# Performance work log

Hardware: AMD Instinct MI355X
Metric: run time of the kernel (lower is better)

Reference implementation:

```python
import jax, jax.numpy as jnp
import numpy as np

N, E, H, NH, RBF = 20000, 200000, 128, 8, 64
HD = H // NH
CUT_HI = 5.0


def _ln(t, s, b, eps=1e-6):
    mu = t.mean(-1, keepdims=True)
    var = ((t - mu) ** 2).mean(-1, keepdims=True)
    return (t - mu) * jax.lax.rsqrt(var + eps) * s + b


def _cutoff(w):
    # cosine cutoff, cutoff_lower = 0
    return 0.5 * (jnp.cos(w * (jnp.pi / CUT_HI)) + 1.0) * (w < CUT_HI)


def _xavier(k, fi, fo):
    lim = float(np.sqrt(6.0 / (fi + fo)))
    return jax.random.uniform(k, (fi, fo), minval=-lim, maxval=lim, dtype=jnp.float32)


def setup_inputs() -> dict:
    key = jax.random.key(0)
    ks = jax.random.split(key, 16)
    return {
        "x": jax.random.normal(ks[0], (N, H), jnp.float32),
        "vec": jax.random.normal(ks[1], (N, 3, H), jnp.float32),
        "edge_weight": jax.random.uniform(ks[2], (E, 1), jnp.float32) * 6.0,
        "edge_attr": jax.random.uniform(ks[3], (E, RBF), jnp.float32),
        "edge_vec": jax.random.normal(ks[4], (E, 3), jnp.float32),
        "senders": jax.random.randint(ks[5], (E,), 0, N, jnp.int32),
        "receivers": jax.random.randint(ks[6], (E,), 0, N, jnp.int32),
        "ln_s": jnp.ones((H,), jnp.float32), "ln_b": jnp.zeros((H,), jnp.float32),
        "Wq": _xavier(ks[7], H, H), "bq": jnp.zeros((H,), jnp.float32),
        "Wk": _xavier(ks[8], H, H), "bk": jnp.zeros((H,), jnp.float32),
        "Wv": _xavier(ks[9], H, 3 * H), "bv": jnp.zeros((3 * H,), jnp.float32),
        "Wvec": _xavier(ks[10], H, 3 * H),
        "Wdk": _xavier(ks[11], RBF, H), "bdk": jnp.zeros((H,), jnp.float32),
        "Wdv": _xavier(ks[12], RBF, 3 * H), "bdv": jnp.zeros((3 * H,), jnp.float32),
        "Wo": _xavier(ks[13], H, 3 * H), "bo": jnp.zeros((3 * H,), jnp.float32),
        "qln_s": jnp.ones((HD,), jnp.float32), "qln_b": jnp.zeros((HD,), jnp.float32),
        "kln_s": jnp.ones((HD,), jnp.float32), "kln_b": jnp.zeros((HD,), jnp.float32),
    }


def reference(x, vec, edge_weight, edge_attr, edge_vec, senders, receivers,
              ln_s, ln_b, Wq, bq, Wk, bk, Wv, bv, Wvec, Wdk, bdk, Wdv, bdv,
              Wo, bo, qln_s, qln_b, kln_s, kln_b):
    act = jax.nn.silu
    n = x.shape[0]
    xn = _ln(x, ln_s, ln_b)                                    # [N,H]
    q = _ln((xn @ Wq + bq).reshape(n, NH, HD), qln_s, qln_b)   # [N,h,d]
    k = _ln((xn @ Wk + bk).reshape(n, NH, HD), kln_s, kln_b)   # [N,h,d]
    v = (xn @ Wv + bv).reshape(n, NH, 3 * HD)                  # [N,h,3d]
    vp = vec @ Wvec                                            # [N,3,3H]
    vec1, vec2, vec3 = jnp.split(vp, 3, axis=-1)               # [N,3,H] each
    vec_dot = (vec1 * vec2).sum(axis=1)                        # [N,H]
    vec_h = vec.reshape(n, 3, NH, HD)                          # [N,3,h,d]
    dk = act(edge_attr @ Wdk + bdk).reshape(-1, NH, HD)        # [E,h,d]
    dv = act(edge_attr @ Wdv + bdv).reshape(-1, NH, 3 * HD)    # [E,h,3d]
    # message
    attn = (q[receivers] * k[senders] * dk).sum(axis=-1)       # [E,h]
    attn = act(attn) * _cutoff(edge_weight)                    # [E,h]
    v_j = v[senders] * dv                                      # [E,h,3d]
    xm, m1, m2 = jnp.split(v_j, 3, axis=2)                     # [E,h,d]
    xm = xm * attn[:, :, None]                                 # [E,h,d]
    vec_m = vec_h[senders] * m1[:, None] + m2[:, None] * edge_vec[:, :, None, None]  # [E,3,h,d]
    # aggregate
    x_agg = jax.ops.segment_sum(xm, receivers, num_segments=n).reshape(n, H)
    vec_agg = jax.ops.segment_sum(vec_m, receivers, num_segments=n).reshape(n, 3, H)
    o1, o2, o3 = jnp.split(x_agg @ Wo + bo, 3, axis=1)         # [N,H] each
    dvec = vec3 * o1[:, None] + vec_agg                        # [N,3,H]
    dx = vec_dot * o2 + o3                                     # [N,H]
    return (dx, dvec)
```

## Files before the change

### kernel.cpp

```cpp
#include <hip/hip_runtime.h>
#include <stdint.h>

#define NN 20000
#define NE 200000

typedef __attribute__((ext_vector_type(8))) short bf16x8;
typedef __attribute__((ext_vector_type(4))) float f32x4;

__device__ __forceinline__ float bf2f(uint32_t u) {
  union { uint32_t i; float f; } v; v.i = u << 16; return v.f;
}
__device__ __forceinline__ uint16_t f2bf(float f) {
  union { float f; uint32_t i; } v; v.f = f;
  return (uint16_t)((v.i + 0x7fffu + ((v.i >> 16) & 1u)) >> 16);
}
__device__ __forceinline__ uint32_t pk2(float lo, float hi) {
  return (uint32_t)f2bf(lo) | ((uint32_t)f2bf(hi) << 16);
}
__device__ __forceinline__ float siluf(float x) { return x / (1.f + __expf(-x)); }
__device__ __forceinline__ float prod2(uint32_t q2, uint32_t k2, uint32_t d2) {
  return bf2f(q2 & 0xffffu) * bf2f(k2 & 0xffffu) * bf2f(d2 & 0xffffu)
       + bf2f(q2 >> 16) * bf2f(k2 >> 16) * bf2f(d2 >> 16);
}

__global__ void k_prep(const float* __restrict__ Wq, const float* __restrict__ Wk,
                       const float* __restrict__ Wv, const float* __restrict__ Wvec,
                       const float* __restrict__ Wdk, const float* __restrict__ Wdv,
                       const float* __restrict__ Wo, const float* __restrict__ bq,
                       const float* __restrict__ bk, const float* __restrict__ bv,
                       const float* __restrict__ bdk, const float* __restrict__ bdv,
                       uint16_t* __restrict__ WTqkv, uint16_t* __restrict__ WTvec,
                       uint16_t* __restrict__ WTdkv2, uint16_t* __restrict__ WTo,
                       float* __restrict__ Bqkv, float* __restrict__ Bdkv2) {
  int idx = blockIdx.x * 256 + threadIdx.x;
  if (idx < 81920) {
    int j = idx;
    float v;
    if (j < 16384)      { int c = j >> 7, k = j & 127; v = Wq[k * 128 + c]; }
    else if (j < 32768) { j -= 16384; int c = j >> 7, k = j & 127; v = Wk[k * 128 + c]; }
    else                { j -= 32768; int c = j >> 7, k = j & 127; v = Wv[k * 384 + c]; }
    WTqkv[idx] = f2bf(v);
    return;
  }
  idx -= 81920;
  if (idx < 49152) {
    int c = idx >> 7, k = idx & 127;
    WTvec[idx] = f2bf(Wvec[k * 384 + c]);
    return;
  }
  idx -= 49152;
  if (idx < 32768) {
    int rr = idx >> 6, k = idx & 63;
    float v;
    if (rr < 128) v = Wdk[k * 128 + rr];
    else {
      int j = rr - 128, p = j >> 7, hd = j & 127;
      int c = (hd >> 4) * 48 + p * 16 + (hd & 15);
      v = Wdv[k * 384 + c];
    }
    WTdkv2[idx] = f2bf(v);
    return;
  }
  idx -= 32768;
  if (idx < 49152) {
    int c = idx >> 7, k = idx & 127;
    WTo[idx] = f2bf(Wo[k * 384 + c]);
    return;
  }
  idx -= 49152;
  if (idx < 640) Bqkv[idx] = (idx < 128) ? bq[idx] : ((idx < 256) ? bk[idx - 128] : bv[idx - 256]);
  else if (idx < 1152) {
    int t = idx - 640;
    if (t < 128) Bdkv2[t] = bdk[t];
    else {
      int j = t - 128, p = j >> 7, hd = j & 127;
      Bdkv2[t] = bdv[(hd >> 4) * 48 + p * 16 + (hd & 15)];
    }
  }
}

__global__ void k_node_pre(const float* __restrict__ x, const float* __restrict__ s,
                           const float* __restrict__ b, const float* __restrict__ vec,
                           uint16_t* __restrict__ xn_b, uint16_t* __restrict__ vec_b) {
  if (blockIdx.x < 5000) {
    int gt = blockIdx.x * 256 + threadIdx.x;
    int node = gt >> 6, lane = gt & 63;
    if (node >= NN) return;
    const float* row = x + (size_t)node * 128;
    float2 v = *(const float2*)&row[lane * 2];
    float sum = v.x + v.y, sq = v.x * v.x + v.y * v.y;
    #pragma unroll
    for (int off = 32; off; off >>= 1) { sum += __shfl_xor(sum, off); sq += __shfl_xor(sq, off); }
    float mu = sum * (1.f / 128.f);
    float var = sq * (1.f / 128.f) - mu * mu;
    float rs = rsqrtf(var + 1e-6f);
    float o0 = (v.x - mu) * rs * s[lane * 2] + b[lane * 2];
    float o1 = (v.y - mu) * rs * s[lane * 2 + 1] + b[lane * 2 + 1];
    ((uint32_t*)xn_b)[(size_t)node * 64 + lane] = pk2(o0, o1);
  } else {
    int i = (blockIdx.x - 5000) * 256 + threadIdx.x;
    if (i >= NN * 3 * 64) return;
    float2 v = ((const float2*)vec)[i];
    ((uint32_t*)vec_b)[i] = pk2(v.x, v.y);
  }
}

__global__ void k_cast_bf16(const float* __restrict__ src, uint16_t* __restrict__ dst, int npairs) {
  int i = blockIdx.x * 256 + threadIdx.x;
  if (i >= npairs) return;
  float2 v = ((const float2*)src)[i];
  ((uint32_t*)dst)[i] = pk2(v.x, v.y);
}

__global__ void k_hist(const int* __restrict__ rcv, int* __restrict__ deg) {
  int e = blockIdx.x * 256 + threadIdx.x;
  if (e < NE) atomicAdd(&deg[rcv[e]], 1);
}

__global__ void k_scan1(const int* __restrict__ deg, int* __restrict__ bsum) {
  __shared__ int ws[4];
  int i = blockIdx.x * 256 + threadIdx.x;
  int x = (i < NN) ? deg[i] : 0;
  #pragma unroll
  for (int d = 32; d; d >>= 1) x += __shfl_xor(x, d);
  if ((threadIdx.x & 63) == 0) ws[threadIdx.x >> 6] = x;
  __syncthreads();
  if (threadIdx.x == 0) bsum[blockIdx.x] = ws[0] + ws[1] + ws[2] + ws[3];
}

__global__ void k_scan2(int* __restrict__ bsum, int nb, int* __restrict__ off) {
  int lane = threadIdx.x;
  int carry = 0;
  for (int base = 0; base < nb; base += 64) {
    int i = base + lane;
    int x = (i < nb) ? bsum[i] : 0;
    int v = x;
    #pragma unroll
    for (int d = 1; d < 64; d <<= 1) { int y = __shfl_up(v, d); if (lane >= d) v += y; }
    if (i < nb) bsum[i] = carry + v - x;
    carry += __shfl(v, 63);
  }
  if (lane == 0) off[NN] = carry;
}

__global__ void k_scan3(const int* __restrict__ deg, const int* __restrict__ bsum,
                        int* __restrict__ off, int* __restrict__ cur) {
  __shared__ int ws[4];
  int t = threadIdx.x, lane = t & 63, w = t >> 6;
  int i = blockIdx.x * 256 + t;
  int x = (i < NN) ? deg[i] : 0;
  int v = x;
  #pragma unroll
  for (int d = 1; d < 64; d <<= 1) { int y = __shfl_up(v, d); if (lane >= d) v += y; }
  if (lane == 63) ws[w] = v;
  __syncthreads();
  int wadd = 0;
  for (int j = 0; j < w; j++) wadd += ws[j];
  int excl = bsum[blockIdx.x] + wadd + v - x;
  if (i < NN) { off[i] = excl; cur[i] = excl; }
}

__global__ void k_scatter(const int* __restrict__ rcv, int* __restrict__ cur,
                          int* __restrict__ perm) {
  int e = blockIdx.x * 256 + threadIdx.x;
  if (e >= NE) return;
  int pos = atomicAdd(&cur[rcv[e]], 1);
  perm[pos] = e;
}

__global__ void k_permute(const int* __restrict__ perm, const int* __restrict__ snd,
                          const int* __restrict__ rcv, const float* __restrict__ ew,
                          const float* __restrict__ evec, int* __restrict__ sndp,
                          int* __restrict__ rcvp, float4* __restrict__ edata) {
  int i = blockIdx.x * 256 + threadIdx.x;
  if (i >= NE) return;
  int e = perm[i];
  sndp[i] = snd[e];
  rcvp[i] = rcv[e];
  float w = ew[e];
  float cut = (w < 5.f) ? 0.5f * (__cosf(w * 0.628318530717958648f) + 1.f) : 0.f;
  edata[i] = make_float4(evec[e * 3], evec[e * 3 + 1], evec[e * 3 + 2], cut);
}

template <int KTOT, bool OUT_BF16, bool SILU>
__global__ __launch_bounds__(256) void k_gemm(const uint16_t* __restrict__ A,
                                              const uint16_t* __restrict__ BT,
                                              const float* __restrict__ bias,
                                              void* __restrict__ Cout, int M, int Fo) {
  __shared__ __align__(16) uint16_t As[128 * 72];
  __shared__ __align__(16) uint16_t Bs[128 * 72];
  int t = threadIdx.x;
  int l = t & 63;
  int row0 = blockIdx.y * 128, col0 = blockIdx.x * 128;
  int wm = ((t >> 6) >> 1) * 64, wn = ((t >> 6) & 1) * 64;
  f32x4 acc[4][4] = {};
  for (int kt = 0; kt < KTOT; kt += 64) {
    __syncthreads();
    #pragma unroll
    for (int i = 0; i < 4; i++) {
      int c = i * 256 + t;
      int row = c >> 3, ko = (c & 7) * 8;
      uint4 av = make_uint4(0u, 0u, 0u, 0u);
      int gr = row0 + row;
      if (gr < M) av = *(const uint4*)&A[(size_t)gr * KTOT + kt + ko];
      *(uint4*)&As[row * 72 + ko] = av;
      uint4 bw = *(const uint4*)&BT[(size_t)(col0 + row) * KTOT + kt + ko];
      *(uint4*)&Bs[row * 72 + ko] = bw;
    }
    __syncthreads();
    #pragma unroll
    for (int kk = 0; kk < 64; kk += 32) {
      bf16x8 af[4], bfr[4];
      #pragma unroll
      for (int mf = 0; mf < 4; mf++)
        af[mf] = *(const bf16x8*)&As[(wm + mf * 16 + (l & 15)) * 72 + (l >> 4) * 8 + kk];
      #pragma unroll
      for (int nf = 0; nf < 4; nf++)
        bfr[nf] = *(const bf16x8*)&Bs[(wn + nf * 16 + (l & 15)) * 72 + (l >> 4) * 8 + kk];
      #pragma unroll
      for (int mf = 0; mf < 4; mf++)
        #pragma unroll
        for (int nf = 0; nf < 4; nf++)
          acc[mf][nf] = __builtin_amdgcn_mfma_f32_16x16x32_bf16(af[mf], bfr[nf], acc[mf][nf], 0, 0, 0);
    }
  }
  float* Cf = (float*)Cout;
  uint16_t* Cb = (uint16_t*)Cout;
  #pragma unroll
  for (int mf = 0; mf < 4; mf++) {
    #pragma unroll
    for (int r = 0; r < 4; r++) {
      int grow = row0 + wm + mf * 16 + (l >> 4) * 4 + r;
      if (grow >= M) continue;
      #pragma unroll
      for (int nf = 0; nf < 4; nf++) {
        int gcol = col0 + wn + nf * 16 + (l & 15);
        float v = acc[mf][nf][r];
        if (bias) v += bias[gcol];
        if (SILU) v = siluf(v);
        if (OUT_BF16) Cb[(size_t)grow * Fo + gcol] = f2bf(v);
        else          Cf[(size_t)grow * Fo + gcol] = v;
      }
    }
  }
}

__global__ void k_headln(const uint16_t* __restrict__ qkv, const float* __restrict__ qs,
                         const float* __restrict__ qb, const float* __restrict__ ks,
                         const float* __restrict__ kb, uint16_t* __restrict__ out) {
  int idx = blockIdx.x * 256 + threadIdx.x;
  if (idx >= NN * 16) return;
  int n = idx >> 4, ph = idx & 15, part = ph >> 3, h = ph & 7;
  const uint16_t* src = qkv + (size_t)n * 640 + part * 128 + h * 16;
  float v[16], sum = 0.f;
  #pragma unroll
  for (int i = 0; i < 16; i++) { v[i] = bf2f(src[i]); sum += v[i]; }
  float mu = sum * (1.f / 16.f), var = 0.f;
  #pragma unroll
  for (int i = 0; i < 16; i++) { float dd = v[i] - mu; var += dd * dd; }
  float rs = rsqrtf(var * (1.f / 16.f) + 1e-6f);
  const float* sc = part ? ks : qs;
  const float* bb = part ? kb : qb;
  uint16_t* dst = out + (size_t)n * 256 + part * 128 + h * 16;
  #pragma unroll
  for (int i = 0; i < 16; i++) dst[i] = f2bf((v[i] - mu) * rs * sc[i] + bb[i]);
}

__device__ __forceinline__ void mfma_cb(const uint16_t* As, const uint16_t* __restrict__ BT2,
                                        int cb, int wn, int l, f32x4 acc[4][2]) {
  #pragma unroll
  for (int kk = 0; kk < 2; kk++) {
    bf16x8 af[4];
    #pragma unroll
    for (int mf = 0; mf < 4; mf++)
      af[mf] = *(const bf16x8*)&As[(mf * 16 + (l & 15)) * 68 + (l >> 4) * 8 + kk * 32];
    #pragma unroll
    for (int nf = 0; nf < 2; nf++) {
      bf16x8 bv = *(const bf16x8*)&BT2[(size_t)(cb * 128 + wn + nf * 16 + (l & 15)) * 64 +
                                       (l >> 4) * 8 + kk * 32];
      #pragma unroll
      for (int mf = 0; mf < 4; mf++)
        acc[mf][nf] = __builtin_amdgcn_mfma_f32_16x16x32_bf16(af[mf], bv, acc[mf][nf], 0, 0, 0);
    }
  }
}

__device__ __forceinline__ void silu_store(uint16_t* mt, const float* bias_l, int cb,
                                           int wn, int l, f32x4 acc[4][2]) {
  #pragma unroll
  for (int mf = 0; mf < 4; mf++)
    #pragma unroll
    for (int r = 0; r < 4; r++) {
      int row = mf * 16 + (l >> 4) * 4 + r;
      #pragma unroll
      for (int nf = 0; nf < 2; nf++) {
        int c = wn + nf * 16 + (l & 15);
        mt[row * 140 + c] = f2bf(siluf(acc[mf][nf][r] + bias_l[cb * 128 + c]));
      }
    }
}

__global__ __launch_bounds__(256) void k_edge_all(
    const float* __restrict__ ea, const int* __restrict__ perm,
    const int* __restrict__ sndp, const int* __restrict__ rcvp,
    const int* __restrict__ off, const float4* __restrict__ edata,
    const uint16_t* __restrict__ WT2, const float* __restrict__ Bd2,
    const uint16_t* __restrict__ qk_b, const uint16_t* __restrict__ qkv_b,
    const uint16_t* __restrict__ vec_b, float* __restrict__ xagg,
    float* __restrict__ vecagg) {
  __shared__ __align__(16) uint16_t As[64 * 68];
  __shared__ __align__(16) uint16_t mt1[64 * 140];
  __shared__ __align__(16) uint16_t mt2[64 * 140];
  __shared__ float attn_l[64 * 8];
  __shared__ float bias_l[512];
  __shared__ int sndl[64], rcvl[64], lo_g[64], hi_g[64];
  __shared__ float4 ed4[64];

  int e0 = blockIdx.x * 64;
  int t = threadIdx.x, l = t & 63, wn = (t >> 6) * 32;

  if (t < 64) {
    int e = e0 + t;
    int s = sndp[e], r = rcvp[e];
    sndl[t] = s; rcvl[t] = r;
    lo_g[t] = off[r]; hi_g[t] = off[r + 1];
    ed4[t] = edata[e];
  }
  bias_l[t] = Bd2[t];
  bias_l[t + 256] = Bd2[t + 256];
  {
    int row = t >> 2, qo = (t & 3) * 16;
    int pe = perm[e0 + row];
    const float* src = ea + (size_t)pe * 64 + qo;
    float4 f0 = *(const float4*)src;
    float4 f1 = *(const float4*)(src + 4);
    float4 f2 = *(const float4*)(src + 8);
    float4 f3 = *(const float4*)(src + 12);
    uint4 o0, o1;
    o0.x = pk2(f0.x, f0.y); o0.y = pk2(f0.z, f0.w);
    o0.z = pk2(f1.x, f1.y); o0.w = pk2(f1.z, f1.w);
    o1.x = pk2(f2.x, f2.y); o1.y = pk2(f2.z, f2.w);
    o1.z = pk2(f3.x, f3.y); o1.w = pk2(f3.z, f3.w);
    *(uint4*)&As[row * 68 + qo] = o0;
    *(uint4*)&As[row * 68 + qo + 8] = o1;
  }
  __syncthreads();

  { f32x4 acc[4][2] = {}; mfma_cb(As, WT2, 0, wn, l, acc); silu_store(mt1, bias_l, 0, wn, l, acc); }
  __syncthreads();

  #pragma unroll
  for (int pass = 0; pass < 2; pass++) {
    int task = pass * 256 + t;
    int el = task >> 3, h = task & 7;
    int rn = rcvl[el], sn = sndl[el];
    const uint32_t* qp = (const uint32_t*)(qk_b + (size_t)rn * 256 + h * 16);
    const uint32_t* kp = (const uint32_t*)(qk_b + (size_t)sn * 256 + 128 + h * 16);
    const uint32_t* dp = (const uint32_t*)&mt1[el * 140 + h * 16];
    float dot = 0.f;
    #pragma unroll
    for (int j = 0; j < 8; j++) dot += prod2(qp[j], kp[j], dp[j]);
    attn_l[el * 8 + h] = siluf(dot) * ed4[el].w;
  }
  __syncthreads();

  { f32x4 acc[4][2] = {}; mfma_cb(As, WT2, 1, wn, l, acc); silu_store(mt1, bias_l, 1, wn, l, acc); }
  __syncthreads();

  {
    int col = t & 127, half = t >> 7;
    int h0 = half * 32, h1 = h0 + 32;
    int voff = 256 + (col >> 4) * 48 + (col & 15);
    float accx = 0.f;
    #pragma unroll 4
    for (int i = h0; i < h1; i++) {
      int n = rcvl[i];
      float m = bf2f(mt1[i * 140 + col]);
      float a = attn_l[i * 8 + (col >> 4)];
      float v0 = bf2f(qkv_b[(size_t)sndl[i] * 640 + voff]);
      accx += v0 * m * a;
      if (i == h1 - 1 || rcvl[i + 1] != n) {
        float* dst = &xagg[(size_t)n * 128 + col];
        if (lo_g[i] >= e0 + h0 && hi_g[i] <= e0 + h1) *dst = accx;
        else atomicAdd(dst, accx);
        accx = 0.f;
      }
    }
  }
  __syncthreads();

  { f32x4 acc[4][2] = {}; mfma_cb(As, WT2, 2, wn, l, acc); silu_store(mt1, bias_l, 2, wn, l, acc); }
  { f32x4 acc[4][2] = {}; mfma_cb(As, WT2, 3, wn, l, acc); silu_store(mt2, bias_l, 3, wn, l, acc); }
  __syncthreads();

  {
    int col = t & 127, half = t >> 7;
    int h0 = half * 32, h1 = h0 + 32;
    int v1o = 256 + (col >> 4) * 48 + 16 + (col & 15);
    float a0 = 0.f, a1 = 0.f, a2 = 0.f;
    #pragma unroll 4
    for (int i = h0; i < h1; i++) {
      int n = rcvl[i];
      int s = sndl[i];
      float m1d = bf2f(mt1[i * 140 + col]);
      float m2d = bf2f(mt2[i * 140 + col]);
      const uint16_t* vb = qkv_b + (size_t)s * 640 + v1o;
      float mm1 = bf2f(vb[0]) * m1d;
      float mm2 = bf2f(vb[16]) * m2d;
      const uint16_t* vv = vec_b + (size_t)s * 384 + col;
      float4 ev = ed4[i];
      a0 += bf2f(vv[0])   * mm1 + ev.x * mm2;
      a1 += bf2f(vv[128]) * mm1 + ev.y * mm2;
      a2 += bf2f(vv[256]) * mm1 + ev.z * mm2;
      if (i == h1 - 1 || rcvl[i + 1] != n) {
        float* d0 = &vecagg[((size_t)n * 3 + 0) * 128 + col];
        float* d1 = &vecagg[((size_t)n * 3 + 1) * 128 + col];
        float* d2 = &vecagg[((size_t)n * 3 + 2) * 128 + col];
        if (lo_g[i] >= e0 + h0 && hi_g[i] <= e0 + h1) { *d0 = a0; *d1 = a1; *d2 = a2; }
        else { atomicAdd(d0, a0); atomicAdd(d1, a1); atomicAdd(d2, a2); }
        a0 = a1 = a2 = 0.f;
      }
    }
  }
}

__global__ void k_final(const float* __restrict__ o, const uint16_t* __restrict__ vp,
                        float* __restrict__ dx, float* __restrict__ dvec) {
  int idx = blockIdx.x * 256 + threadIdx.x;
  if (idx >= NN * 128) return;
  int n = idx >> 7, j = idx & 127;
  const float* op = o + (size_t)n * 384;
  float o1 = op[j], o2 = op[128 + j], o3 = op[256 + j];
  const uint16_t* vpn = vp + (size_t)n * 3 * 384;
  float vd = 0.f;
  #pragma unroll
  for (int c = 0; c < 3; c++)
    vd += bf2f(vpn[c * 384 + j]) * bf2f(vpn[c * 384 + 128 + j]);
  dx[idx] = vd * o2 + o3;
  #pragma unroll
  for (int c = 0; c < 3; c++) {
    size_t vi = ((size_t)n * 3 + c) * 128 + j;
    dvec[vi] = bf2f(vpn[c * 384 + 256 + j]) * o1 + dvec[vi];
  }
}

static inline int cdiv_i(long long a, long long b) { return (int)((a + b - 1) / b); }

extern "C" void kernel_launch(void* const* d_in, const int* in_sizes, int n_in,
                              void* d_out, int out_size, void* d_ws, size_t ws_size,
                              hipStream_t stream) {
  const float* x    = (const float*)d_in[0];
  const float* vec  = (const float*)d_in[1];
  const float* ew   = (const float*)d_in[2];
  const float* ea   = (const float*)d_in[3];
  const float* evec = (const float*)d_in[4];
  const int*   snd  = (const int*)d_in[5];
  const int*   rcv  = (const int*)d_in[6];
  const float* ln_s = (const float*)d_in[7];
  const float* ln_b = (const float*)d_in[8];
  const float* Wq = (const float*)d_in[9];   const float* bq = (const float*)d_in[10];
  const float* Wk = (const float*)d_in[11];  const float* bk = (const float*)d_in[12];
  const float* Wv = (const float*)d_in[13];  const float* bv = (const float*)d_in[14];
  const float* Wvec = (const float*)d_in[15];
  const float* Wdk = (const float*)d_in[16]; const float* bdk = (const float*)d_in[17];
  const float* Wdv = (const float*)d_in[18]; const float* bdv = (const float*)d_in[19];
  const float* Wo = (const float*)d_in[20];  const float* bo = (const float*)d_in[21];
  const float* qln_s = (const float*)d_in[22]; const float* qln_b = (const float*)d_in[23];
  const float* kln_s = (const float*)d_in[24]; const float* kln_b = (const float*)d_in[25];
  (void)in_sizes; (void)n_in; (void)ws_size;

  uint8_t* p = (uint8_t*)d_ws;
  auto alloc = [&](size_t bytes) -> uint8_t* {
    uint8_t* r = p; p += (bytes + 255) & ~(size_t)255; return r;
  };
  uint16_t* WTqkv = (uint16_t*)alloc(640 * 128 * 2);
  float*    Bqkv  = (float*)alloc(640 * 4);
  uint16_t* WTvec = (uint16_t*)alloc(384 * 128 * 2);
  uint16_t* WTdkv = (uint16_t*)alloc(512 * 64 * 2);
  float*    Bdkv  = (float*)alloc(512 * 4);
  uint16_t* WTo   = (uint16_t*)alloc(384 * 128 * 2);
  int*      deg   = (int*)alloc(NN * 4);
  int*      off   = (int*)alloc((NN + 1) * 4);
  int*      cur   = (int*)alloc(NN * 4);
  int*      bsum  = (int*)alloc(256 * 4);
  int*      perm  = (int*)alloc((size_t)NE * 4);
  int*      sndp  = (int*)alloc((size_t)NE * 4);
  int*      rcvp  = (int*)alloc((size_t)NE * 4);
  float4*   edata = (float4*)alloc((size_t)NE * 16);
  uint16_t* xn_b  = (uint16_t*)alloc((size_t)NN * 128 * 2);
  uint16_t* qkv_b = (uint16_t*)alloc((size_t)NN * 640 * 2);
  uint16_t* qk_b  = (uint16_t*)alloc((size_t)NN * 256 * 2);
  uint16_t* vec_b = (uint16_t*)alloc((size_t)NN * 3 * 128 * 2);
  uint16_t* vp    = (uint16_t*)alloc((size_t)NN * 3 * 384 * 2);
  float*    o      = (float*)alloc((size_t)NN * 384 * 4);
  uint16_t* xagg_b = (uint16_t*)alloc((size_t)NN * 128 * 2);

  float* xagg   = (float*)d_out;
  float* vecagg = (float*)d_out + (size_t)NN * 128;

  hipMemsetAsync(d_out, 0, (size_t)out_size * 4, stream);

  k_prep<<<cdiv_i(81920 + 49152 + 32768 + 49152 + 1152, 256), 256, 0, stream>>>(
      Wq, Wk, Wv, Wvec, Wdk, Wdv, Wo, bq, bk, bv, bdk, bdv,
      WTqkv, WTvec, WTdkv, WTo, Bqkv, Bdkv);

  int NSB = cdiv_i(NN, 256);
  hipMemsetAsync(deg, 0, NN * 4, stream);
  k_hist<<<cdiv_i(NE, 256), 256, 0, stream>>>(rcv, deg);
  k_scan1<<<NSB, 256, 0, stream>>>(deg, bsum);
  k_scan2<<<1, 64, 0, stream>>>(bsum, NSB, off);
  k_scan3<<<NSB, 256, 0, stream>>>(deg, bsum, off, cur);
  k_scatter<<<cdiv_i(NE, 256), 256, 0, stream>>>(rcv, cur, perm);
  k_permute<<<cdiv_i(NE, 256), 256, 0, stream>>>(perm, snd, rcv, ew, evec, sndp, rcvp, edata);

  k_node_pre<<<5000 + cdiv_i((long long)NN * 3 * 64, 256), 256, 0, stream>>>(
      x, ln_s, ln_b, vec, xn_b, vec_b);

  { dim3 g(640 / 128, cdiv_i(NN, 128));
    k_gemm<128, true, false><<<g, 256, 0, stream>>>(xn_b, WTqkv, Bqkv, qkv_b, NN, 640); }
  k_headln<<<cdiv_i((long long)NN * 16, 256), 256, 0, stream>>>(qkv_b, qln_s, qln_b, kln_s, kln_b, qk_b);

  { dim3 g(384 / 128, cdiv_i((long long)NN * 3, 128));
    k_gemm<128, true, false><<<g, 256, 0, stream>>>(vec_b, WTvec, nullptr, vp, NN * 3, 384); }

  k_edge_all<<<NE / 64, 256, 0, stream>>>(ea, perm, sndp, rcvp, off, edata, WTdkv, Bdkv,
                                          qk_b, qkv_b, vec_b, xagg, vecagg);

  k_cast_bf16<<<cdiv_i((long long)NN * 64, 256), 256, 0, stream>>>(xagg, xagg_b, NN * 64);
  { dim3 g(384 / 128, cdiv_i(NN, 128));
    k_gemm<128, false, false><<<g, 256, 0, stream>>>(xagg_b, WTo, bo, o, NN, 384); }

  k_final<<<cdiv_i((long long)NN * 128, 256), 256, 0, stream>>>(o, vp, xagg, vecagg);
}
```

Baseline: 369.7 us.

## Pre-permute edge_attr to bf16 and process edge tile in two 32-row halves

The permute kernel now gathers edge_attr by the sorted edge order and converts it to bf16 in a contiguous buffer, so the fused edge kernel loads its A tile with coalesced 16-byte reads instead of a per-row gather of fp32 data. The edge kernel processes its 64 edges as two 32-row halves, which shrinks the message tiles in shared memory, drops the shared bias array in favor of per-lane bias registers, and should allow more blocks per CU. The cost is an extra pass that writes and rereads a 25 MB bf16 buffer, more barriers per block, and more partial-segment atomics because the aggregation segments are shorter.

```diff
diff --git a/kernel.cpp b/kernel.cpp
--- a/kernel.cpp
+++ b/kernel.cpp
@@ -168,18 +168,27 @@
   perm[pos] = e;
 }
 
-__global__ void k_permute(const int* __restrict__ perm, const int* __restrict__ snd,
-                          const int* __restrict__ rcv, const float* __restrict__ ew,
-                          const float* __restrict__ evec, int* __restrict__ sndp,
+__global__ void k_permute(const float* __restrict__ ea, const int* __restrict__ perm,
+                          const int* __restrict__ snd, const int* __restrict__ rcv,
+                          const float* __restrict__ ew, const float* __restrict__ evec,
+                          uint16_t* __restrict__ ea_perm, int* __restrict__ sndp,
                           int* __restrict__ rcvp, float4* __restrict__ edata) {
-  int i = blockIdx.x * 256 + threadIdx.x;
-  if (i >= NE) return;
+  int idx = blockIdx.x * 256 + threadIdx.x;
+  if (idx >= NE * 16) return;
+  int i = idx >> 4, j = idx & 15;
   int e = perm[i];
-  sndp[i] = snd[e];
-  rcvp[i] = rcv[e];
-  float w = ew[e];
-  float cut = (w < 5.f) ? 0.5f * (__cosf(w * 0.628318530717958648f) + 1.f) : 0.f;
-  edata[i] = make_float4(evec[e * 3], evec[e * 3 + 1], evec[e * 3 + 2], cut);
+  float4 v = *(const float4*)&ea[(size_t)e * 64 + j * 4];
+  uint2 o;
+  o.x = pk2(v.x, v.y);
+  o.y = pk2(v.z, v.w);
+  *(uint2*)&ea_perm[(size_t)i * 64 + j * 4] = o;
+  if (j == 0) {
+    sndp[i] = snd[e];
+    rcvp[i] = rcv[e];
+    float w = ew[e];
+    float cut = (w < 5.f) ? 0.5f * (__cosf(w * 0.628318530717958648f) + 1.f) : 0.f;
+    edata[i] = make_float4(evec[e * 3], evec[e * 3 + 1], evec[e * 3 + 2], cut);
+  }
 }
 
 template <int KTOT, bool OUT_BF16, bool SILU>
@@ -266,53 +275,52 @@
   for (int i = 0; i < 16; i++) dst[i] = f2bf((v[i] - mu) * rs * sc[i] + bb[i]);
 }
 
-__device__ __forceinline__ void mfma_cb(const uint16_t* As, const uint16_t* __restrict__ BT2,
-                                        int cb, int wn, int l, f32x4 acc[4][2]) {
+__device__ __forceinline__ void mfma32(const uint16_t* As, int r0,
+                                       const uint16_t* __restrict__ BT2, int cb,
+                                       int wn, int l, f32x4 acc[2][2]) {
   #pragma unroll
   for (int kk = 0; kk < 2; kk++) {
-    bf16x8 af[4];
-    #pragma unroll
-    for (int mf = 0; mf < 4; mf++)
-      af[mf] = *(const bf16x8*)&As[(mf * 16 + (l & 15)) * 68 + (l >> 4) * 8 + kk * 32];
+    bf16x8 af[2];
+    #pragma unroll
+    for (int mf = 0; mf < 2; mf++)
+      af[mf] = *(const bf16x8*)&As[(r0 + mf * 16 + (l & 15)) * 68 + (l >> 4) * 8 + kk * 32];
     #pragma unroll
     for (int nf = 0; nf < 2; nf++) {
       bf16x8 bv = *(const bf16x8*)&BT2[(size_t)(cb * 128 + wn + nf * 16 + (l & 15)) * 64 +
                                        (l >> 4) * 8 + kk * 32];
       #pragma unroll
-      for (int mf = 0; mf < 4; mf++)
+      for (int mf = 0; mf < 2; mf++)
         acc[mf][nf] = __builtin_amdgcn_mfma_f32_16x16x32_bf16(af[mf], bv, acc[mf][nf], 0, 0, 0);
     }
   }
 }
 
-__device__ __forceinline__ void silu_store(uint16_t* mt, const float* bias_l, int cb,
-                                           int wn, int l, f32x4 acc[4][2]) {
-  #pragma unroll
-  for (int mf = 0; mf < 4; mf++)
+__device__ __forceinline__ void silu_store32(uint16_t* mt, const float* bsv,
+                                             int wn, int l, f32x4 acc[2][2]) {
+  #pragma unroll
+  for (int mf = 0; mf < 2; mf++)
     #pragma unroll
     for (int r = 0; r < 4; r++) {
       int row = mf * 16 + (l >> 4) * 4 + r;
       #pragma unroll
       for (int nf = 0; nf < 2; nf++) {
         int c = wn + nf * 16 + (l & 15);
-        mt[row * 140 + c] = f2bf(siluf(acc[mf][nf][r] + bias_l[cb * 128 + c]));
+        mt[row * 140 + c] = f2bf(siluf(acc[mf][nf][r] + bsv[nf]));
       }
     }
 }
 
 __global__ __launch_bounds__(256) void k_edge_all(
-    const float* __restrict__ ea, const int* __restrict__ perm,
-    const int* __restrict__ sndp, const int* __restrict__ rcvp,
-    const int* __restrict__ off, const float4* __restrict__ edata,
-    const uint16_t* __restrict__ WT2, const float* __restrict__ Bd2,
-    const uint16_t* __restrict__ qk_b, const uint16_t* __restrict__ qkv_b,
-    const uint16_t* __restrict__ vec_b, float* __restrict__ xagg,
-    float* __restrict__ vecagg) {
+    const uint16_t* __restrict__ eap, const int* __restrict__ sndp,
+    const int* __restrict__ rcvp, const int* __restrict__ off,
+    const float4* __restrict__ edata, const uint16_t* __restrict__ WT2,
+    const float* __restrict__ Bd2, const uint16_t* __restrict__ qk_b,
+    const uint16_t* __restrict__ qkv_b, const uint16_t* __restrict__ vec_b,
+    float* __restrict__ xagg, float* __restrict__ vecagg) {
   __shared__ __align__(16) uint16_t As[64 * 68];
-  __shared__ __align__(16) uint16_t mt1[64 * 140];
-  __shared__ __align__(16) uint16_t mt2[64 * 140];
-  __shared__ float attn_l[64 * 8];
-  __shared__ float bias_l[512];
+  __shared__ __align__(16) uint16_t mtA[32 * 140];
+  __shared__ __align__(16) uint16_t mtB[32 * 140];
+  __shared__ float attn_l[32 * 8];
   __shared__ int sndl[64], rcvl[64], lo_g[64], hi_g[64];
   __shared__ float4 ed4[64];
 
@@ -321,106 +329,99 @@
 
   if (t < 64) {
     int e = e0 + t;
-    int s = sndp[e], r = rcvp[e];
-    sndl[t] = s; rcvl[t] = r;
+    int r = rcvp[e];
+    sndl[t] = sndp[e]; rcvl[t] = r;
     lo_g[t] = off[r]; hi_g[t] = off[r + 1];
     ed4[t] = edata[e];
   }
-  bias_l[t] = Bd2[t];
-  bias_l[t + 256] = Bd2[t + 256];
-  {
-    int row = t >> 2, qo = (t & 3) * 16;
-    int pe = perm[e0 + row];
-    const float* src = ea + (size_t)pe * 64 + qo;
-    float4 f0 = *(const float4*)src;
-    float4 f1 = *(const float4*)(src + 4);
-    float4 f2 = *(const float4*)(src + 8);
-    float4 f3 = *(const float4*)(src + 12);
-    uint4 o0, o1;
-    o0.x = pk2(f0.x, f0.y); o0.y = pk2(f0.z, f0.w);
-    o0.z = pk2(f1.x, f1.y); o0.w = pk2(f1.z, f1.w);
-    o1.x = pk2(f2.x, f2.y); o1.y = pk2(f2.z, f2.w);
-    o1.z = pk2(f3.x, f3.y); o1.w = pk2(f3.z, f3.w);
-    *(uint4*)&As[row * 68 + qo] = o0;
-    *(uint4*)&As[row * 68 + qo + 8] = o1;
+  #pragma unroll
+  for (int i = 0; i < 2; i++) {
+    int c = i * 256 + t;
+    int row = c >> 3, ko = (c & 7) * 8;
+    *(uint4*)&As[row * 68 + ko] = *(const uint4*)&eap[(size_t)(e0 + row) * 64 + ko];
+  }
+  float bs[4][2];
+  #pragma unroll
+  for (int cb = 0; cb < 4; cb++) {
+    bs[cb][0] = Bd2[cb * 128 + wn + (l & 15)];
+    bs[cb][1] = Bd2[cb * 128 + wn + 16 + (l & 15)];
   }
   __syncthreads();
 
-  { f32x4 acc[4][2] = {}; mfma_cb(As, WT2, 0, wn, l, acc); silu_store(mt1, bias_l, 0, wn, l, acc); }
-  __syncthreads();
-
-  #pragma unroll
-  for (int pass = 0; pass < 2; pass++) {
-    int task = pass * 256 + t;
-    int el = task >> 3, h = task & 7;
-    int rn = rcvl[el], sn = sndl[el];
-    const uint32_t* qp = (const uint32_t*)(qk_b + (size_t)rn * 256 + h * 16);
-    const uint32_t* kp = (const uint32_t*)(qk_b + (size_t)sn * 256 + 128 + h * 16);
-    const uint32_t* dp = (const uint32_t*)&mt1[el * 140 + h * 16];
-    float dot = 0.f;
-    #pragma unroll
-    for (int j = 0; j < 8; j++) dot += prod2(qp[j], kp[j], dp[j]);
-    attn_l[el * 8 + h] = siluf(dot) * ed4[el].w;
-  }
-  __syncthreads();
-
-  { f32x4 acc[4][2] = {}; mfma_cb(As, WT2, 1, wn, l, acc); silu_store(mt1, bias_l, 1, wn, l, acc); }
-  __syncthreads();
-
-  {
-    int col = t & 127, half = t >> 7;
-    int h0 = half * 32, h1 = h0 + 32;
-    int voff = 256 + (col >> 4) * 48 + (col & 15);
-    float accx = 0.f;
-    #pragma unroll 4
-    for (int i = h0; i < h1; i++) {
-      int n = rcvl[i];
-      float m = bf2f(mt1[i * 140 + col]);
-      float a = attn_l[i * 8 + (col >> 4)];
-      float v0 = bf2f(qkv_b[(size_t)sndl[i] * 640 + voff]);
-      accx += v0 * m * a;
-      if (i == h1 - 1 || rcvl[i + 1] != n) {
-        float* dst = &xagg[(size_t)n * 128 + col];
-        if (lo_g[i] >= e0 + h0 && hi_g[i] <= e0 + h1) *dst = accx;
-        else atomicAdd(dst, accx);
-        accx = 0.f;
+  #pragma unroll
+  for (int half = 0; half < 2; half++) {
+    int r0 = half * 32;
+    { f32x4 acc[2][2] = {}; mfma32(As, r0, WT2, 0, wn, l, acc); silu_store32(mtA, bs[0], wn, l, acc); }
+    __syncthreads();
+    {
+      int el = t >> 3, h = t & 7;
+      int ge = r0 + el;
+      int rn = rcvl[ge], sn = sndl[ge];
+      const uint32_t* qp = (const uint32_t*)(qk_b + (size_t)rn * 256 + h * 16);
+      const uint32_t* kp = (const uint32_t*)(qk_b + (size_t)sn * 256 + 128 + h * 16);
+      const uint32_t* dp = (const uint32_t*)&mtA[el * 140 + h * 16];
+      float dot = 0.f;
+      #pragma unroll
+      for (int j = 0; j < 8; j++) dot += prod2(qp[j], kp[j], dp[j]);
+      attn_l[el * 8 + h] = siluf(dot) * ed4[ge].w;
+    }
+    __syncthreads();
+    { f32x4 acc[2][2] = {}; mfma32(As, r0, WT2, 1, wn, l, acc); silu_store32(mtA, bs[1], wn, l, acc); }
+    __syncthreads();
+    {
+      int col = t & 127, sub = t >> 7;
+      int i0 = r0 + sub * 16, i1 = i0 + 16;
+      int voff = 256 + (col >> 4) * 48 + (col & 15);
+      float accx = 0.f;
+      #pragma unroll 8
+      for (int i = i0; i < i1; i++) {
+        int n = rcvl[i];
+        float m = bf2f(mtA[(i - r0) * 140 + col]);
+        float a = attn_l[(i - r0) * 8 + (col >> 4)];
+        float v0 = bf2f(qkv_b[(size_t)sndl[i] * 640 + voff]);
+        accx += v0 * m * a;
+        if (i == i1 - 1 || rcvl[i + 1] != n) {
+          float* dst = &xagg[(size_t)n * 128 + col];
+          if (lo_g[i] >= e0 + i0 && hi_g[i] <= e0 + i1) *dst = accx;
+          else atomicAdd(dst, accx);
+          accx = 0.f;
+        }
       }
     }
-  }
-  __syncthreads();
-
-  { f32x4 acc[4][2] = {}; mfma_cb(As, WT2, 2, wn, l, acc); silu_store(mt1, bias_l, 2, wn, l, acc); }
-  { f32x4 acc[4][2] = {}; mfma_cb(As, WT2, 3, wn, l, acc); silu_store(mt2, bias_l, 3, wn, l, acc); }
-  __syncthreads();
-
-  {
-    int col = t & 127, half = t >> 7;
-    int h0 = half * 32, h1 = h0 + 32;
-    int v1o = 256 + (col >> 4) * 48 + 16 + (col & 15);
-    float a0 = 0.f, a1 = 0.f, a2 = 0.f;
-    #pragma unroll 4
-    for (int i = h0; i < h1; i++) {
-      int n = rcvl[i];
-      int s = sndl[i];
-      float m1d = bf2f(mt1[i * 140 + col]);
-      float m2d = bf2f(mt2[i * 140 + col]);
-      const uint16_t* vb = qkv_b + (size_t)s * 640 + v1o;
-      float mm1 = bf2f(vb[0]) * m1d;
-      float mm2 = bf2f(vb[16]) * m2d;
-      const uint16_t* vv = vec_b + (size_t)s * 384 + col;
-      float4 ev = ed4[i];
-      a0 += bf2f(vv[0])   * mm1 + ev.x * mm2;
-      a1 += bf2f(vv[128]) * mm1 + ev.y * mm2;
-      a2 += bf2f(vv[256]) * mm1 + ev.z * mm2;
-      if (i == h1 - 1 || rcvl[i + 1] != n) {
-        float* d0 = &vecagg[((size_t)n * 3 + 0) * 128 + col];
-        float* d1 = &vecagg[((size_t)n * 3 + 1) * 128 + col];
-        float* d2 = &vecagg[((size_t)n * 3 + 2) * 128 + col];
-        if (lo_g[i] >= e0 + h0 && hi_g[i] <= e0 + h1) { *d0 = a0; *d1 = a1; *d2 = a2; }
-        else { atomicAdd(d0, a0); atomicAdd(d1, a1); atomicAdd(d2, a2); }
-        a0 = a1 = a2 = 0.f;
+    __syncthreads();
+    { f32x4 acc[2][2] = {}; mfma32(As, r0, WT2, 2, wn, l, acc); silu_store32(mtA, bs[2], wn, l, acc); }
+    { f32x4 acc[2][2] = {}; mfma32(As, r0, WT2, 3, wn, l, acc); silu_store32(mtB, bs[3], wn, l, acc); }
+    __syncthreads();
+    {
+      int col = t & 127, sub = t >> 7;
+      int i0 = r0 + sub * 16, i1 = i0 + 16;
+      int v1o = 256 + (col >> 4) * 48 + 16 + (col & 15);
+      float a0 = 0.f, a1 = 0.f, a2 = 0.f;
+      #pragma unroll 8
+      for (int i = i0; i < i1; i++) {
+        int n = rcvl[i];
+        int s = sndl[i];
+        float m1d = bf2f(mtA[(i - r0) * 140 + col]);
+        float m2d = bf2f(mtB[(i - r0) * 140 + col]);
+        const uint16_t* vb = qkv_b + (size_t)s * 640 + v1o;
+        float mm1 = bf2f(vb[0]) * m1d;
+        float mm2 = bf2f(vb[16]) * m2d;
+        const uint16_t* vv = vec_b + (size_t)s * 384 + col;
+        float4 ev = ed4[i];
+        a0 += bf2f(vv[0])   * mm1 + ev.x * mm2;
+        a1 += bf2f(vv[128]) * mm1 + ev.y * mm2;
+        a2 += bf2f(vv[256]) * mm1 + ev.z * mm2;
+        if (i == i1 - 1 || rcvl[i + 1] != n) {
+          float* d0 = &vecagg[((size_t)n * 3 + 0) * 128 + col];
+          float* d1 = &vecagg[((size_t)n * 3 + 1) * 128 + col];
+          float* d2 = &vecagg[((size_t)n * 3 + 2) * 128 + col];
+          if (lo_g[i] >= e0 + i0 && hi_g[i] <= e0 + i1) { *d0 = a0; *d1 = a1; *d2 = a2; }
+          else { atomicAdd(d0, a0); atomicAdd(d1, a1); atomicAdd(d2, a2); }
+          a0 = a1 = a2 = 0.f;
+        }
       }
     }
+    __syncthreads();
   }
 }
 
@@ -487,6 +488,7 @@
   int*      sndp  = (int*)alloc((size_t)NE * 4);
   int*      rcvp  = (int*)alloc((size_t)NE * 4);
   float4*   edata = (float4*)alloc((size_t)NE * 16);
+  uint16_t* ea_perm = (uint16_t*)alloc((size_t)NE * 64 * 2);
   uint16_t* xn_b  = (uint16_t*)alloc((size_t)NN * 128 * 2);
   uint16_t* qkv_b = (uint16_t*)alloc((size_t)NN * 640 * 2);
   uint16_t* qk_b  = (uint16_t*)alloc((size_t)NN * 256 * 2);
@@ -511,7 +513,8 @@
   k_scan2<<<1, 64, 0, stream>>>(bsum, NSB, off);
   k_scan3<<<NSB, 256, 0, stream>>>(deg, bsum, off, cur);
   k_scatter<<<cdiv_i(NE, 256), 256, 0, stream>>>(rcv, cur, perm);
-  k_permute<<<cdiv_i(NE, 256), 256, 0, stream>>>(perm, snd, rcv, ew, evec, sndp, rcvp, edata);
+  k_permute<<<cdiv_i((long long)NE * 16, 256), 256, 0, stream>>>(ea, perm, snd, rcv, ew, evec,
+                                                                 ea_perm, sndp, rcvp, edata);
 
   k_node_pre<<<5000 + cdiv_i((long long)NN * 3 * 64, 256), 256, 0, stream>>>(
       x, ln_s, ln_b, vec, xn_b, vec_b);
@@ -523,7 +526,7 @@
   { dim3 g(384 / 128, cdiv_i((long long)NN * 3, 128));
     k_gemm<128, true, false><<<g, 256, 0, stream>>>(vec_b, WTvec, nullptr, vp, NN * 3, 384); }
 
-  k_edge_all<<<NE / 64, 256, 0, stream>>>(ea, perm, sndp, rcvp, off, edata, WTdkv, Bdkv,
+  k_edge_all<<<NE / 64, 256, 0, stream>>>(ea_perm, sndp, rcvp, off, edata, WTdkv, Bdkv,
                                           qk_b, qkv_b, vec_b, xagg, vecagg);
 
   k_cast_bf16<<<cdiv_i((long long)NN * 64, 256), 256, 0, stream>>>(xagg, xagg_b, NN * 64);
```

Measured after the change: 361.9 us. -2.1%, faster.
